# Performance work log

Measured on AMD Instinct MI355X. Metric: run time of the kernel, lower is better.

## Reference

```python
import jax, jax.numpy as jnp
import numpy as np

N, E, F = 50000, 500000, 32
H, C = 4, 64          # nheads, graph_hidden_channels
NHID, NOUT, B = 256, 256, 1000


def setup_inputs() -> dict:
    key = jax.random.key(0)
    ks = jax.random.split(key, 24)
    s = 0.05
    inp = {
        "x": jax.random.normal(ks[0], (N, F), jnp.float32),
        "edge_index": jax.random.randint(ks[1], (2, E), 0, N, jnp.int64),
        "batch": jnp.sort(jax.random.randint(ks[2], (N,), 0, B, jnp.int64)),
        # conv1: F -> H*C
        "W1": jax.random.normal(ks[3], (F, H * C), jnp.float32) * s,
        "a_src1": jax.random.normal(ks[4], (H, C), jnp.float32) * s,
        "a_dst1": jax.random.normal(ks[5], (H, C), jnp.float32) * s,
        "b1": jnp.zeros((H * C,), jnp.float32),
        # conv2: H*C -> H*C
        "W2": jax.random.normal(ks[6], (H * C, H * C), jnp.float32) * s,
        "a_src2": jax.random.normal(ks[7], (H, C), jnp.float32) * s,
        "a_dst2": jax.random.normal(ks[8], (H, C), jnp.float32) * s,
        "b2": jnp.zeros((H * C,), jnp.float32),
        # conv3: H*C -> C, heads=1
        "W3": jax.random.normal(ks[9], (H * C, C), jnp.float32) * s,
        "a_src3": jax.random.normal(ks[10], (1, C), jnp.float32) * s,
        "a_dst3": jax.random.normal(ks[11], (1, C), jnp.float32) * s,
        "b3": jnp.zeros((C,), jnp.float32),
        # MLP head + LayerNorm
        "Wm1": jax.random.normal(ks[12], (C, NHID), jnp.float32) * s,
        "bm1": jnp.zeros((NHID,), jnp.float32),
        "Wm2": jax.random.normal(ks[13], (NHID, NOUT), jnp.float32) * s,
        "bm2": jnp.zeros((NOUT,), jnp.float32),
        "g2": jnp.ones((NOUT,), jnp.float32),
        "be2": jnp.zeros((NOUT,), jnp.float32),
    }
    return inp


def _gat_conv(x, ei, W, a_src, a_dst, bias, heads, ch):
    """PyG GATConv: linear -> per-edge leaky_relu attention -> segment softmax
    over incoming edges of each dst node -> scatter-add aggregation."""
    n = x.shape[0]
    h = (x @ W).reshape(n, heads, ch)                     # [N,H,C]
    src, dst = ei[0], ei[1]
    al_s = jnp.sum(h * a_src, axis=-1)                    # [N,H]
    al_d = jnp.sum(h * a_dst, axis=-1)                    # [N,H]
    e = jax.nn.leaky_relu(al_s[src] + al_d[dst], 0.2)     # [E,H]
    m = jax.ops.segment_max(e, dst, num_segments=n)       # stable softmax
    p = jnp.exp(e - m[dst])
    z = jax.ops.segment_sum(p, dst, num_segments=n)
    alpha = p / (z[dst] + 1e-16)                          # [E,H]
    out = jax.ops.segment_sum(alpha[:, :, None] * h[src], dst, num_segments=n)
    return out.reshape(n, heads * ch) + bias


def _layer_norm(x, g, b, eps=1e-5):
    mu = jnp.mean(x, axis=-1, keepdims=True)
    v = jnp.var(x, axis=-1, keepdims=True)
    return (x - mu) * jax.lax.rsqrt(v + eps) * g + b


def reference(x, edge_index, batch, W1, a_src1, a_dst1, b1, W2, a_src2, a_dst2, b2,
              W3, a_src3, a_dst3, b3, Wm1, bm1, Wm2, bm2, g2, be2):
    n = x.shape[0]
    loops = jnp.tile(jnp.arange(n, dtype=edge_index.dtype)[None, :], (2, 1))
    ei = jnp.concatenate([edge_index, loops], axis=1)     # add_self_loops=True
    h1 = jax.nn.relu(_gat_conv(x, ei, W1, a_src1, a_dst1, b1, H, C))
    h2 = jax.nn.relu(_gat_conv(h1, ei, W2, a_src2, a_dst2, b2, H, C))
    h3 = _gat_conv(h2, ei, W3, a_src3, a_dst3, b3, 1, C)  # [N,C]
    cnt = jax.ops.segment_sum(jnp.ones((n,), h3.dtype), batch, num_segments=B)
    xg = jax.ops.segment_sum(h3, batch, num_segments=B) / jnp.maximum(cnt, 1.0)[:, None]
    y = jax.nn.relu(xg @ Wm1 + bm1)
    y = y @ Wm2 + bm2
    return _layer_norm(y, g2, be2)
```

## Files before the change

kernel.cpp:

```cpp
#include <hip/hip_runtime.h>
#include <hip/hip_bf16.h>

#define N_NODES 50000
#define N_PAD 50176
#define N_EDGES 500000
#define E2_EDGES 550000
#define F_IN 32
#define HEADS 4
#define CH 64
#define HC 256
#define NB 1000
#define NHID 256
#define NOUT 256
#define SLOT_CAP 64

static inline int cdiv(long long a, long long b) { return (int)((a + b - 1) / b); }

typedef __bf16 bf16x8 __attribute__((ext_vector_type(8)));
typedef unsigned short us8 __attribute__((ext_vector_type(8)));
typedef float f32x4 __attribute__((ext_vector_type(4)));
union BU { us8 u; bf16x8 b; };

__device__ inline unsigned short f2bf(float f) {
    unsigned u = __float_as_uint(f);
    return (unsigned short)((u + 0x7fffu + ((u >> 16) & 1u)) >> 16);
}
__device__ inline float bf2f(unsigned short h) {
    return __uint_as_float(((unsigned)h) << 16);
}

__device__ inline void wconv_one(const float* __restrict__ W,
                                 unsigned short* __restrict__ Wf_hi,
                                 unsigned short* __restrict__ Wf_lo,
                                 int K, int M, int idx) {
    int k = idx / M, m = idx % M;
    float v = W[idx];
    unsigned short hi = f2bf(v);
    unsigned short lo = f2bf(v - bf2f(hi));
    int tcol = m >> 4, l16 = m & 15;
    int ch = k >> 5, quad = (k >> 3) & 3, j = k & 7;
    int NCH = K >> 5;
    size_t dst = ((((size_t)tcol * NCH + ch) * 64) + quad * 16 + l16) * 8 + j;
    Wf_hi[dst] = hi;
    Wf_lo[dst] = lo;
}

#define PREP_T0 N_NODES
#define PREP_T1 (PREP_T0 + N_NODES * F_IN)
#define PREP_T2 (PREP_T1 + F_IN * HC)
#define PREP_T3 (PREP_T2 + HC * HC)
#define PREP_T4 (PREP_T3 + HC * CH)
__global__ void prep_kernel(const float* __restrict__ x,
                            unsigned short* __restrict__ xh,
                            unsigned short* __restrict__ xl,
                            const float* __restrict__ W1,
                            unsigned short* __restrict__ wt1h, unsigned short* __restrict__ wt1l,
                            const float* __restrict__ W2,
                            unsigned short* __restrict__ wt2h, unsigned short* __restrict__ wt2l,
                            const float* __restrict__ W3,
                            unsigned short* __restrict__ wt3h, unsigned short* __restrict__ wt3l,
                            int* __restrict__ deg) {
    int t = blockIdx.x * blockDim.x + threadIdx.x;
    if (t < PREP_T0) {
        deg[t] = 0;
    } else if (t < PREP_T1) {
        int i = t - PREP_T0;
        int node = i / F_IN, c = i % F_IN;
        float v = x[i];
        unsigned short hi = f2bf(v);
        size_t dst = (((size_t)(node >> 4)) * 64 + ((c >> 3) & 3) * 16 + (node & 15)) * 8 + (c & 7);
        xh[dst] = hi;
        xl[dst] = f2bf(v - bf2f(hi));
    } else if (t < PREP_T2) {
        wconv_one(W1, wt1h, wt1l, F_IN, HC, t - PREP_T1);
    } else if (t < PREP_T3) {
        wconv_one(W2, wt2h, wt2l, HC, HC, t - PREP_T2);
    } else if (t < PREP_T4) {
        wconv_one(W3, wt3h, wt3l, HC, CH, t - PREP_T3);
    }
}


__device__ __forceinline__ void scatter_tile(int t, const int* __restrict__ ei,
                                             int* __restrict__ deg,
                                             unsigned short* __restrict__ slots) {
    int e = t * 256 + threadIdx.x;
    if (e >= E2_EDGES) return;
    int s, d;
    if (e < N_EDGES) { s = ei[e]; d = ei[N_EDGES + e]; }
    else             { s = d = e - N_EDGES; }
    int pos = atomicAdd(deg + d, 1);
    if (pos < SLOT_CAP) slots[(d << 6) + pos] = (unsigned short)s;
}

template<int K, int M, bool ALO>
__device__ __forceinline__ void gemm_tile(
    int bid,
    const unsigned short* __restrict__ Ah, const unsigned short* __restrict__ Al,
    const unsigned short* __restrict__ Wf_hi, const unsigned short* __restrict__ Wf_lo,
    const float* __restrict__ a_src, const float* __restrict__ a_dst,
    unsigned short* __restrict__ Hout, float* __restrict__ als,
    float* __restrict__ ald, int n_rows) {
    constexpr int NCH = K / 32;
    constexpr int CW = M / 64;
    constexpr int RW = 4 / CW;
    constexpr int H_ = M / 64;
    const int wave = threadIdx.x >> 6, lane = threadIdx.x & 63;
    const int quad = lane >> 4, l16 = lane & 15;
    const int head = wave % CW;
    const int col0 = head * 64;
    const int row0 = bid * (RW * 64) + (wave / CW) * 64;
    const int rt0 = row0 >> 4;

    f32x4 acc[4][4];
#pragma unroll
    for (int rs = 0; rs < 4; rs++)
#pragma unroll
        for (int t = 0; t < 4; t++) acc[rs][t] = (f32x4){0.f, 0.f, 0.f, 0.f};

    const unsigned short* aph[4];
    const unsigned short* apl[4];
#pragma unroll
    for (int rs = 0; rs < 4; rs++) {
        size_t off = (((size_t)(rt0 + rs) * NCH) * 64 + lane) * 8;
        aph[rs] = Ah + off;
        if (ALO) apl[rs] = Al + off;
    }
    const unsigned short* bh = Wf_hi + ((size_t)(col0 >> 4) * NCH * 64 + lane) * 8;
    const unsigned short* bl = Wf_lo + ((size_t)(col0 >> 4) * NCH * 64 + lane) * 8;

#pragma unroll
    for (int ch = 0; ch < NCH; ch++) {
        BU a_h[4], a_l[4], b_h[4], b_l[4];
#pragma unroll
        for (int rs = 0; rs < 4; rs++) {
            a_h[rs].u = *(const us8*)(aph[rs] + ch * 512);
            if (ALO) a_l[rs].u = *(const us8*)(apl[rs] + ch * 512);
        }
#pragma unroll
        for (int t = 0; t < 4; t++) {
            b_h[t].u = *(const us8*)(bh + (size_t)(t * NCH + ch) * 512);
            b_l[t].u = *(const us8*)(bl + (size_t)(t * NCH + ch) * 512);
        }
#pragma unroll
        for (int t = 0; t < 4; t++) {
#pragma unroll
            for (int rs = 0; rs < 4; rs++) {
                acc[rs][t] = __builtin_amdgcn_mfma_f32_16x16x32_bf16(a_h[rs].b, b_h[t].b, acc[rs][t], 0, 0, 0);
                acc[rs][t] = __builtin_amdgcn_mfma_f32_16x16x32_bf16(a_h[rs].b, b_l[t].b, acc[rs][t], 0, 0, 0);
                if (ALO)
                    acc[rs][t] = __builtin_amdgcn_mfma_f32_16x16x32_bf16(a_l[rs].b, b_h[t].b, acc[rs][t], 0, 0, 0);
            }
        }
    }

    float sv[4], dv[4];
#pragma unroll
    for (int t = 0; t < 4; t++) {
        sv[t] = a_src[col0 + t * 16 + l16];
        dv[t] = a_dst[col0 + t * 16 + l16];
    }
#pragma unroll
    for (int rs = 0; rs < 4; rs++) {
        const int orow0 = row0 + rs * 16 + quad * 4;
#pragma unroll
        for (int i = 0; i < 4; i++) {
            int r = orow0 + i;
            bool ok = (r < n_rows);
            float ps = 0.f, pd = 0.f;
#pragma unroll
            for (int t = 0; t < 4; t++) {
                float v = acc[rs][t][i];
                ps += v * sv[t];
                pd += v * dv[t];
                if (ok) Hout[(size_t)r * M + col0 + t * 16 + l16] = f2bf(v);
            }
            ps += __shfl_xor(ps, 1);  pd += __shfl_xor(pd, 1);
            ps += __shfl_xor(ps, 2);  pd += __shfl_xor(pd, 2);
            ps += __shfl_xor(ps, 4);  pd += __shfl_xor(pd, 4);
            ps += __shfl_xor(ps, 8);  pd += __shfl_xor(pd, 8);
            if (l16 == 0 && ok) {
                als[r * H_ + head] = ps;
                ald[r * H_ + head] = pd;
            }
        }
    }
}

#define NT_G1 ((N_NODES + 63) / 64)
#define NT_SC ((E2_EDGES + 255) / 256)

__global__ __launch_bounds__(256) void gemm1_scatter_kernel(
    const unsigned short* __restrict__ Ah, const unsigned short* __restrict__ Al,
    const unsigned short* __restrict__ Wf_hi, const unsigned short* __restrict__ Wf_lo,
    const float* __restrict__ a_src, const float* __restrict__ a_dst,
    unsigned short* __restrict__ Hout, float* __restrict__ als,
    float* __restrict__ ald,
    const int* __restrict__ ei, int* __restrict__ deg,
    unsigned short* __restrict__ slots) {
    if (blockIdx.x < NT_G1)
        gemm_tile<F_IN, HC, true>(blockIdx.x, Ah, Al, Wf_hi, Wf_lo, a_src, a_dst,
                                  Hout, als, ald, N_NODES);
    else
        scatter_tile(blockIdx.x - NT_G1, ei, deg, slots);
}

template<int K, int M, bool ALO>
__global__ __launch_bounds__(256) void mfma_lin_fused_kernel(
    const unsigned short* __restrict__ Ah, const unsigned short* __restrict__ Al,
    const unsigned short* __restrict__ Wf_hi, const unsigned short* __restrict__ Wf_lo,
    const float* __restrict__ a_src, const float* __restrict__ a_dst,
    unsigned short* __restrict__ Hout, float* __restrict__ als,
    float* __restrict__ ald, int n_rows) {
    gemm_tile<K, M, ALO>(blockIdx.x, Ah, Al, Wf_hi, Wf_lo, a_src, a_dst, Hout, als, ald, n_rows);
}

__global__ __launch_bounds__(256, 4) void gat_agg_v3_kernel(
    const unsigned short* __restrict__ slots, const int* __restrict__ deg,
    const unsigned short* __restrict__ h,
    const float* __restrict__ als, const float* __restrict__ ald,
    const float* __restrict__ bias, unsigned short* __restrict__ outh) {
    constexpr int LP = 264;
    __shared__ unsigned short smh[16 * LP];
    const int tid = threadIdx.x;
    const int wave = tid >> 6, lane = tid & 63;
    const int cl = lane & 31, half = lane >> 5;
    const int head = cl >> 3;
    const int rt = blockIdx.x;

    float bv[8];
#pragma unroll
    for (int i = 0; i < 8; i++) bv[i] = bias[cl * 8 + i];

    const int nb = rt * 16 + wave * 4;
    int lenv[4];
    float adv[4];
#pragma unroll
    for (int nn = 0; nn < 4; nn++) {
        lenv[nn] = min(deg[nb + nn], SLOT_CAP);
        adv[nn] = ald[((nb + nn) << 2) + head];
    }
    const unsigned short* hp = h + cl * 8;

    for (int nn = 0; nn < 4; nn++) {
        const int len = lenv[nn];
        const int lm = len - 1;
        const int base = (nb + nn) << 6;
        const float ad = adv[nn];
        float z = 0.f;
        float a[8];
#pragma unroll
        for (int i = 0; i < 8; i++) a[i] = 0.f;
        for (int k = 0; k < len; k += 16) {
            int ss[8];
#pragma unroll
            for (int j = 0; j < 8; j++) {
                int ii = min(k + 2 * j + half, lm);
                ss[j] = (int)slots[base + ii];
            }
            __builtin_amdgcn_sched_barrier(0);
            us8 hv[8];
            float alv[8];
#pragma unroll
            for (int j = 0; j < 8; j++) {
                hv[j] = *(const us8*)(hp + ((size_t)ss[j] << 8));
                alv[j] = als[(ss[j] << 2) + head];
            }
            __builtin_amdgcn_sched_barrier(0);
            float p[8];
#pragma unroll
            for (int j = 0; j < 8; j++) {
                float x = alv[j] + ad;
                x = (x > 0.f) ? x : 0.2f * x;
                int e = k + 2 * j + half;
                p[j] = (e < len) ? __expf(x) : 0.f;
                z += p[j];
            }
#pragma unroll
            for (int j = 0; j < 8; j++)
#pragma unroll
                for (int i = 0; i < 8; i++)
                    a[i] += p[j] * bf2f(hv[j][i]);
        }
        z += __shfl_xor(z, 32);
#pragma unroll
        for (int i = 0; i < 8; i++) a[i] += __shfl_xor(a[i], 32);
        if (half == 0) {
            float inv = 1.f / (z + 1e-16f);
            us8 vh;
#pragma unroll
            for (int i = 0; i < 8; i++) {
                float v = fmaxf(a[i] * inv + bv[i], 0.f);
                vh[i] = f2bf(v);
            }
            int nl = wave * 4 + nn;
            *(us8*)(smh + nl * LP + cl * 8) = vh;
        }
    }
    __syncthreads();
#pragma unroll
    for (int f = tid; f < 512; f += 256) {
        int chunk = f >> 6, ln2 = f & 63;
        int quad = ln2 >> 4, l16 = ln2 & 15;
        us8 vh = *(const us8*)(smh + l16 * LP + chunk * 32 + quad * 8);
        size_t dst = (((size_t)rt * 8 + chunk) * 64 + ln2) * 8;
        *(us8*)(outh + dst) = vh;
    }
}

__global__ __launch_bounds__(256) void gat_agg_h1_kernel(
    const unsigned short* __restrict__ slots, const int* __restrict__ deg,
    const unsigned short* __restrict__ h,
    const float* __restrict__ als, const float* __restrict__ ald,
    const float* __restrict__ bias, float* __restrict__ out, int n) {
    const int wave = threadIdx.x >> 6, lane = threadIdx.x & 63;
    const int eg = lane >> 3, cg = lane & 7;
    const int node = (blockIdx.x << 2) + wave;
    if (node >= n) return;
    const int base = node << 6;
    const int len = min(deg[node], SLOT_CAP);
    const float ad = ald[node];
    float z = 0.f;
    float a[8];
#pragma unroll
    for (int i = 0; i < 8; i++) a[i] = 0.f;
    const unsigned short* hp = h + cg * 8;
    for (int k = 0; k < len; k += 8) {
        int e = k + eg;
        int s0 = (int)slots[base + min(e, len - 1)];
        us8 hv = *(const us8*)(hp + ((size_t)s0 << 6));
        float x = als[s0] + ad;
        x = (x > 0.f) ? x : 0.2f * x;
        float p = (e < len) ? __expf(x) : 0.f;
        z += p;
#pragma unroll
        for (int i = 0; i < 8; i++) a[i] += p * bf2f(hv[i]);
    }
#pragma unroll
    for (int off = 8; off <= 32; off <<= 1) {
        z += __shfl_xor(z, off);
#pragma unroll
        for (int i = 0; i < 8; i++) a[i] += __shfl_xor(a[i], off);
    }
    if (eg == 0) {
        float inv = 1.f / (z + 1e-16f);
        float* op = out + ((size_t)node << 6) + cg * 8;
        float4 o0, o1;
        o0.x = a[0] * inv + bias[cg * 8 + 0];
        o0.y = a[1] * inv + bias[cg * 8 + 1];
        o0.z = a[2] * inv + bias[cg * 8 + 2];
        o0.w = a[3] * inv + bias[cg * 8 + 3];
        o1.x = a[4] * inv + bias[cg * 8 + 4];
        o1.y = a[5] * inv + bias[cg * 8 + 5];
        o1.z = a[6] * inv + bias[cg * 8 + 6];
        o1.w = a[7] * inv + bias[cg * 8 + 7];
        *(float4*)op = o0;
        *(float4*)(op + 4) = o1;
    }
}

__global__ __launch_bounds__(256) void head_fused_kernel(
    const float* __restrict__ h3, const int* __restrict__ batch,
    const float* __restrict__ Wm1, const float* __restrict__ bm1,
    const float* __restrict__ Wm2, const float* __restrict__ bm2,
    const float* __restrict__ g2, const float* __restrict__ be2,
    float* __restrict__ out) {
    const int b = blockIdx.x;
    const int tid = threadIdx.x;
    int lo = 0, hi = N_NODES;
    while (lo < hi) { int mid = (lo + hi) >> 1; if (batch[mid] < b) lo = mid + 1; else hi = mid; }
    const int start = lo;
    hi = N_NODES;
    while (lo < hi) { int mid = (lo + hi) >> 1; if (batch[mid] < b + 1) lo = mid + 1; else hi = mid; }
    const int end = lo;

    __shared__ float pr[4][CH];
    __shared__ float xg[CH];
    __shared__ float yr[NHID];
    const int j = tid & 63, g = tid >> 6;
    float s = 0.f;
    for (int n = start + g; n < end; n += 4) s += h3[(size_t)n * CH + j];
    pr[g][j] = s;
    __syncthreads();
    if (tid < CH) {
        float t = pr[0][tid] + pr[1][tid] + pr[2][tid] + pr[3][tid];
        xg[tid] = t / fmaxf((float)(end - start), 1.f);
    }
    __syncthreads();
    float acc1 = bm1[tid];
#pragma unroll 8
    for (int k = 0; k < CH; k++) acc1 += xg[k] * Wm1[(size_t)k * NHID + tid];
    yr[tid] = fmaxf(acc1, 0.f);
    __syncthreads();
    float acc = bm2[tid];
#pragma unroll 8
    for (int k = 0; k < NHID; k++) acc += yr[k] * Wm2[(size_t)k * NOUT + tid];
    float ss = acc, s2 = acc * acc;
    for (int o = 32; o > 0; o >>= 1) {
        ss += __shfl_down(ss, o);
        s2 += __shfl_down(s2, o);
    }
    __shared__ float red[8];
    __shared__ float mv[2];
    int wave = tid >> 6, lane = tid & 63;
    if (lane == 0) { red[wave] = ss; red[4 + wave] = s2; }
    __syncthreads();
    if (tid == 0) {
        float ts = red[0] + red[1] + red[2] + red[3];
        float ts2 = red[4] + red[5] + red[6] + red[7];
        float mu = ts / (float)NOUT;
        float var = ts2 / (float)NOUT - mu * mu;
        mv[0] = mu;
        mv[1] = rsqrtf(var + 1e-5f);
    }
    __syncthreads();
    out[(size_t)b * NOUT + tid] = (acc - mv[0]) * mv[1] * g2[tid] + be2[tid];
}

extern "C" void kernel_launch(void* const* d_in, const int* in_sizes, int n_in,
                              void* d_out, int out_size, void* d_ws, size_t ws_size,
                              hipStream_t stream) {
    const float* x      = (const float*)d_in[0];
    const int*   ei     = (const int*)d_in[1];
    const int*   batch  = (const int*)d_in[2];
    const float* W1     = (const float*)d_in[3];
    const float* as1    = (const float*)d_in[4];
    const float* ad1    = (const float*)d_in[5];
    const float* b1     = (const float*)d_in[6];
    const float* W2     = (const float*)d_in[7];
    const float* as2    = (const float*)d_in[8];
    const float* ad2    = (const float*)d_in[9];
    const float* b2     = (const float*)d_in[10];
    const float* W3     = (const float*)d_in[11];
    const float* as3    = (const float*)d_in[12];
    const float* ad3    = (const float*)d_in[13];
    const float* b3     = (const float*)d_in[14];
    const float* Wm1    = (const float*)d_in[15];
    const float* bm1    = (const float*)d_in[16];
    const float* Wm2    = (const float*)d_in[17];
    const float* bm2    = (const float*)d_in[18];
    const float* g2     = (const float*)d_in[19];
    const float* be2    = (const float*)d_in[20];
    float* out = (float*)d_out;

    unsigned short* bufH = (unsigned short*)d_ws;
    unsigned short* aggh = bufH + (size_t)N_NODES * HC;
    float* bufO3 = (float*)aggh;
    unsigned short* xh   = aggh + (size_t)N_PAD * HC;
    unsigned short* xl   = xh + (size_t)N_PAD * F_IN;
    unsigned short* slots = xl + (size_t)N_PAD * F_IN;
    float* als   = (float*)(slots + (size_t)N_NODES * SLOT_CAP);
    float* ald   = als + (size_t)N_NODES * HEADS;
    int* deg     = (int*)(ald + (size_t)N_NODES * HEADS);
    unsigned short* wt1h = (unsigned short*)(deg + N_NODES);
    unsigned short* wt1l = wt1h + 256 * 32;
    unsigned short* wt2h = wt1l + 256 * 32;
    unsigned short* wt2l = wt2h + 256 * 256;
    unsigned short* wt3h = wt2l + 256 * 256;
    unsigned short* wt3l = wt3h + 64 * 256;

    const int BLK = 256;

    prep_kernel<<<cdiv(PREP_T4, BLK), BLK, 0, stream>>>(
        x, xh, xl, W1, wt1h, wt1l, W2, wt2h, wt2l, W3, wt3h, wt3l, deg);

    gemm1_scatter_kernel<<<NT_G1 + NT_SC, 256, 0, stream>>>(
        xh, xl, wt1h, wt1l, as1, ad1, bufH, als, ald, ei, deg, slots);

    gat_agg_v3_kernel<<<N_NODES / 16, 256, 0, stream>>>(
        slots, deg, bufH, als, ald, b1, aggh);

    mfma_lin_fused_kernel<HC, HC, false><<<cdiv(N_NODES, 64), 256, 0, stream>>>(
        aggh, nullptr, wt2h, wt2l, as2, ad2, bufH, als, ald, N_NODES);
    gat_agg_v3_kernel<<<N_NODES / 16, 256, 0, stream>>>(
        slots, deg, bufH, als, ald, b2, aggh);

    mfma_lin_fused_kernel<HC, CH, false><<<cdiv(N_NODES, 256), 256, 0, stream>>>(
        aggh, nullptr, wt3h, wt3l, as3, ad3, bufH, als, ald, N_NODES);
    gat_agg_h1_kernel<<<cdiv(N_NODES, 4), 256, 0, stream>>>(
        slots, deg, bufH, als, ald, b3, bufO3, N_NODES);

    head_fused_kernel<<<NB, 256, 0, stream>>>(
        bufO3, batch, Wm1, bm1, Wm2, bm2, g2, be2, out);
}
```

Baseline: 318.8 us.

## Fuse layer-3 GAT aggregation into per-graph pooling and MLP head kernel

```diff
diff --git a/kernel.cpp b/kernel.cpp
--- a/kernel.cpp
+++ b/kernel.cpp
@@ -308,83 +308,77 @@
     }
 }
 
-__global__ __launch_bounds__(256) void gat_agg_h1_kernel(
+__global__ __launch_bounds__(256) void agg3_head_kernel(
     const unsigned short* __restrict__ slots, const int* __restrict__ deg,
     const unsigned short* __restrict__ h,
     const float* __restrict__ als, const float* __restrict__ ald,
-    const float* __restrict__ bias, float* __restrict__ out, int n) {
-    const int wave = threadIdx.x >> 6, lane = threadIdx.x & 63;
-    const int eg = lane >> 3, cg = lane & 7;
-    const int node = (blockIdx.x << 2) + wave;
-    if (node >= n) return;
-    const int base = node << 6;
-    const int len = min(deg[node], SLOT_CAP);
-    const float ad = ald[node];
-    float z = 0.f;
-    float a[8];
-#pragma unroll
-    for (int i = 0; i < 8; i++) a[i] = 0.f;
-    const unsigned short* hp = h + cg * 8;
-    for (int k = 0; k < len; k += 8) {
-        int e = k + eg;
-        int s0 = (int)slots[base + min(e, len - 1)];
-        us8 hv = *(const us8*)(hp + ((size_t)s0 << 6));
-        float x = als[s0] + ad;
-        x = (x > 0.f) ? x : 0.2f * x;
-        float p = (e < len) ? __expf(x) : 0.f;
-        z += p;
-#pragma unroll
-        for (int i = 0; i < 8; i++) a[i] += p * bf2f(hv[i]);
-    }
-#pragma unroll
-    for (int off = 8; off <= 32; off <<= 1) {
-        z += __shfl_xor(z, off);
-#pragma unroll
-        for (int i = 0; i < 8; i++) a[i] += __shfl_xor(a[i], off);
-    }
-    if (eg == 0) {
-        float inv = 1.f / (z + 1e-16f);
-        float* op = out + ((size_t)node << 6) + cg * 8;
-        float4 o0, o1;
-        o0.x = a[0] * inv + bias[cg * 8 + 0];
-        o0.y = a[1] * inv + bias[cg * 8 + 1];
-        o0.z = a[2] * inv + bias[cg * 8 + 2];
-        o0.w = a[3] * inv + bias[cg * 8 + 3];
-        o1.x = a[4] * inv + bias[cg * 8 + 4];
-        o1.y = a[5] * inv + bias[cg * 8 + 5];
-        o1.z = a[6] * inv + bias[cg * 8 + 6];
-        o1.w = a[7] * inv + bias[cg * 8 + 7];
-        *(float4*)op = o0;
-        *(float4*)(op + 4) = o1;
-    }
-}
-
-__global__ __launch_bounds__(256) void head_fused_kernel(
-    const float* __restrict__ h3, const int* __restrict__ batch,
+    const float* __restrict__ b3, const int* __restrict__ batch,
     const float* __restrict__ Wm1, const float* __restrict__ bm1,
     const float* __restrict__ Wm2, const float* __restrict__ bm2,
     const float* __restrict__ g2, const float* __restrict__ be2,
     float* __restrict__ out) {
     const int b = blockIdx.x;
     const int tid = threadIdx.x;
+    const int wave = tid >> 6, lane = tid & 63;
+    const int eg = lane >> 3, cg = lane & 7;
+
     int lo = 0, hi = N_NODES;
     while (lo < hi) { int mid = (lo + hi) >> 1; if (batch[mid] < b) lo = mid + 1; else hi = mid; }
     const int start = lo;
     hi = N_NODES;
     while (lo < hi) { int mid = (lo + hi) >> 1; if (batch[mid] < b + 1) lo = mid + 1; else hi = mid; }
     const int end = lo;
-
-    __shared__ float pr[4][CH];
+    const int cnt = end - start;
+
+    __shared__ float wsum[4][CH];
     __shared__ float xg[CH];
     __shared__ float yr[NHID];
-    const int j = tid & 63, g = tid >> 6;
-    float s = 0.f;
-    for (int n = start + g; n < end; n += 4) s += h3[(size_t)n * CH + j];
-    pr[g][j] = s;
+    __shared__ float red[8];
+    __shared__ float mv[2];
+    wsum[wave][lane & 63] = 0.f;
+
+    float asum[8];
+#pragma unroll
+    for (int i = 0; i < 8; i++) asum[i] = 0.f;
+    const unsigned short* hp = h + cg * 8;
+
+    for (int node = start + wave; node < end; node += 4) {
+        const int base = node << 6;
+        const int len = min(deg[node], SLOT_CAP);
+        const float ad = ald[node];
+        float z = 0.f;
+        float a[8];
+#pragma unroll
+        for (int i = 0; i < 8; i++) a[i] = 0.f;
+        for (int k = 0; k < len; k += 8) {
+            int e = k + eg;
+            int s0 = (int)slots[base + min(e, len - 1)];
+            us8 hv = *(const us8*)(hp + ((size_t)s0 << 6));
+            float x = als[s0] + ad;
+            x = (x > 0.f) ? x : 0.2f * x;
+            float p = (e < len) ? __expf(x) : 0.f;
+            z += p;
+#pragma unroll
+            for (int i = 0; i < 8; i++) a[i] += p * bf2f(hv[i]);
+        }
+#pragma unroll
+        for (int off = 8; off <= 32; off <<= 1) {
+            z += __shfl_xor(z, off);
+#pragma unroll
+            for (int i = 0; i < 8; i++) a[i] += __shfl_xor(a[i], off);
+        }
+        float inv = 1.f / (z + 1e-16f);
+#pragma unroll
+        for (int i = 0; i < 8; i++) asum[i] += a[i] * inv;
+    }
+    if (eg == 0) {
+#pragma unroll
+        for (int i = 0; i < 8; i++) wsum[wave][cg * 8 + i] = asum[i];
+    }
     __syncthreads();
     if (tid < CH) {
-        float t = pr[0][tid] + pr[1][tid] + pr[2][tid] + pr[3][tid];
-        xg[tid] = t / fmaxf((float)(end - start), 1.f);
+        float t = wsum[0][tid] + wsum[1][tid] + wsum[2][tid] + wsum[3][tid];
+        xg[tid] = t / fmaxf((float)cnt, 1.f) + b3[tid];
     }
     __syncthreads();
     float acc1 = bm1[tid];
@@ -400,10 +394,7 @@
         ss += __shfl_down(ss, o);
         s2 += __shfl_down(s2, o);
     }
-    __shared__ float red[8];
-    __shared__ float mv[2];
-    int wave = tid >> 6, lane = tid & 63;
-    if (lane == 0) { red[wave] = ss; red[4 + wave] = s2; }
+    if ((tid & 63) == 0) { red[wave] = ss; red[4 + wave] = s2; }
     __syncthreads();
     if (tid == 0) {
         float ts = red[0] + red[1] + red[2] + red[3];
@@ -445,7 +436,6 @@
 
     unsigned short* bufH = (unsigned short*)d_ws;
     unsigned short* aggh = bufH + (size_t)N_NODES * HC;
-    float* bufO3 = (float*)aggh;
     unsigned short* xh   = aggh + (size_t)N_PAD * HC;
     unsigned short* xl   = xh + (size_t)N_PAD * F_IN;
     unsigned short* slots = xl + (size_t)N_PAD * F_IN;
@@ -477,9 +467,7 @@
 
     mfma_lin_fused_kernel<HC, CH, false><<<cdiv(N_NODES, 256), 256, 0, stream>>>(
         aggh, nullptr, wt3h, wt3l, as3, ad3, bufH, als, ald, N_NODES);
-    gat_agg_h1_kernel<<<cdiv(N_NODES, 4), 256, 0, stream>>>(
-        slots, deg, bufH, als, ald, b3, bufO3, N_NODES);
-
-    head_fused_kernel<<<NB, 256, 0, stream>>>(
-        bufO3, batch, Wm1, bm1, Wm2, bm2, g2, be2, out);
-}
+
+    agg3_head_kernel<<<NB, 256, 0, stream>>>(
+        slots, deg, bufH, als, ald, b3, batch, Wm1, bm1, Wm2, bm2, g2, be2, out);
+}
```

Measured after the change: 325.4 us. 1.02x slower.
